# Performance work log

Hardware: AMD Instinct MI355X
Metric: run time of the kernel (lower is better)

## Reference

```python
import jax, jax.numpy as jnp
import numpy as np

K_STE = 10.0
T_STE = 0.1
BN_EPS = 1e-5


def binary_quantize(x):
    # forward of IR-Net BinaryQuantize: sign (sign(0)=0, matching torch.sign)
    return jnp.sign(x)


def setup_inputs() -> dict:
    key = jax.random.key(0)
    k1, k2, k3, k4 = jax.random.split(key, 4)
    B, Cin, Cout, H, W = 32, 256, 256, 56, 56
    x = jax.random.normal(k1, (B, Cin, H, W), dtype=jnp.float32)
    weight = jax.random.normal(k2, (Cout, Cin, 3, 3), dtype=jnp.float32) * 0.05
    gamma = jnp.ones((Cout,), dtype=jnp.float32)
    beta = jnp.zeros((Cout,), dtype=jnp.float32)
    running_mean = jax.random.normal(k3, (Cout,), dtype=jnp.float32) * 0.1
    running_var = jax.random.uniform(k4, (Cout,), dtype=jnp.float32, minval=0.5, maxval=1.5)
    return {"x": x, "weight": weight, "gamma": gamma, "beta": beta,
            "running_mean": running_mean, "running_var": running_var}


def reference(x, weight, gamma, beta, running_mean, running_var):
    stride = 1
    cout = weight.shape[0]
    wf = weight.reshape(cout, -1)                      # [Cout, Cin*3*3]
    n = wf.shape[1]
    mean = jnp.mean(wf, axis=1, keepdims=True)
    # torch std: unbiased (ddof=1)
    std = jnp.sqrt(jnp.sum((wf - mean) ** 2, axis=1, keepdims=True) / (n - 1))
    bw = (wf - mean) / std                             # standardized weights
    # detached per-channel power-of-two scale
    sw = jnp.exp2(jnp.round(jnp.log2(jnp.mean(jnp.abs(bw), axis=1))))  # [Cout]
    sw = jax.lax.stop_gradient(sw)
    bw = binary_quantize(bw).reshape(weight.shape) * sw[:, None, None, None]
    ba = binary_quantize(x)
    y = jax.lax.conv_general_dilated(
        ba, bw, window_strides=(stride, stride), padding=((1, 1), (1, 1)),
        dimension_numbers=("NCHW", "OIHW", "NCHW"))
    # BatchNorm2d (inference) + Hardtanh
    inv = gamma / jnp.sqrt(running_var + BN_EPS)
    y = y * inv[None, :, None, None] + (beta - running_mean * inv)[None, :, None, None]
    return jnp.clip(y, -1.0, 1.0)
```

## Files before the change

### kernel.cpp

```cpp
#include <hip/hip_runtime.h>
#include <hip/hip_bf16.h>
#include <cstdint>
#include <cstddef>


typedef int int4v __attribute__((ext_vector_type(4)));

#define CIN   256
#define COUT  256
#define SPAT  3136
#define SPAD  3364
#define BATCH 32
#define XHALF 32768

__global__ __launch_bounds__(256) void prep_kernel(
    const float* __restrict__ x, int8_t* __restrict__ xp,
    const float* __restrict__ wgt, const float* __restrict__ gamma,
    const float* __restrict__ beta, const float* __restrict__ rmean,
    const float* __restrict__ rvar, int8_t* __restrict__ wfrag,
    float* __restrict__ Sc, float* __restrict__ Tc) {
  const int bx  = blockIdx.x;
  const int by  = blockIdx.y;
  const int tid = threadIdx.x;

  if (bx < 49) {
    const int s0 = bx * 64;
    __shared__ uint8_t xt[64][272];
    const int g  = tid >> 6;
    const int si = tid & 63;
#pragma unroll
    for (int k = 0; k < 4; ++k) {
      const int cin16 = (g * 4 + k) * 16;
      const float* src = x + ((size_t)by * CIN + cin16) * SPAT + s0 + si;
      uint32_t w[4] = {0u, 0u, 0u, 0u};
#pragma unroll
      for (int e = 0; e < 16; ++e) {
        float v = src[(size_t)e * SPAT];
        uint32_t sb = (v > 0.f) ? 1u : ((v < 0.f) ? 0xFFu : 0u);
        w[e >> 2] |= sb << ((e & 3) * 8);
      }
      *(int4v*)&xt[si][cin16] = (int4v){(int)w[0], (int)w[1], (int)w[2], (int)w[3]};
    }
    __syncthreads();
    const int row = tid >> 2;
    const int sub = tid & 3;
    const int s = s0 + row;
    const int h = s / 56;
    int8_t* dst = xp + ((size_t)by * SPAD + (size_t)(s + 2 * h + 59)) * CIN + sub * 64;
#pragma unroll
    for (int j = 0; j < 4; ++j)
      *(int4v*)(dst + j * 16) = *(const int4v*)&xt[row][sub * 64 + j * 16];
    return;
  }

  if (bx == 49) {
    int8_t* xpb = xp + (size_t)by * SPAD * CIN;
    const int4v zz = (int4v){0, 0, 0, 0};
    for (int q = tid; q < 228 * 16; q += 256) {
      int p = q >> 4, c = q & 15;
      int pp;
      if (p < 58)       pp = p;
      else if (p < 116) pp = 57 * 58 + (p - 58);
      else if (p < 172) pp = (p - 116 + 1) * 58;
      else              pp = (p - 172 + 1) * 58 + 57;
      *(int4v*)(xpb + (size_t)pp * CIN + c * 16) = zz;
    }
    return;
  }

  const int co = (bx - 50) * 32 + by;
  __shared__ float red[256];
  const float* wc = wgt + (size_t)co * 2304;
  float v[9];
#pragma unroll
  for (int j = 0; j < 9; ++j) v[j] = wc[tid + j * 256];
  float s = 0.f;
#pragma unroll
  for (int j = 0; j < 9; ++j) s += v[j];
  red[tid] = s; __syncthreads();
#pragma unroll
  for (int o = 128; o > 0; o >>= 1) { if (tid < o) red[tid] += red[tid + o]; __syncthreads(); }
  const float mean = red[0] * (1.0f / 2304.0f);
  __syncthreads();
  float ss = 0.f, sa = 0.f;
#pragma unroll
  for (int j = 0; j < 9; ++j) {
    float d = v[j] - mean;
    ss += d * d;
    sa += fabsf(d);
  }
  red[tid] = ss; __syncthreads();
#pragma unroll
  for (int o = 128; o > 0; o >>= 1) { if (tid < o) red[tid] += red[tid + o]; __syncthreads(); }
  const float var_sum = red[0];
  __syncthreads();
  red[tid] = sa; __syncthreads();
#pragma unroll
  for (int o = 128; o > 0; o >>= 1) { if (tid < o) red[tid] += red[tid + o]; __syncthreads(); }
  const float abs_sum = red[0];
  const float stdv = sqrtf(var_sum / 2303.0f);
  const float mean_abs = abs_sum / (2304.0f * stdv);
  const float sw = exp2f(rintf(log2f(mean_abs)));

  const int z = co >> 7, row = co & 127;
  const int wv = row >> 6, m = (row >> 4) & 3, l15w = row & 15;
#pragma unroll
  for (int j = 0; j < 9; ++j) {
    int i = tid + j * 256;
    int cin = i / 9;
    int tap = i - cin * 9;
    float d = v[j] - mean;
    int8_t bits = (d > 0.f) ? (int8_t)1 : ((d < 0.f) ? (int8_t)-1 : (int8_t)0);
    int c0i = cin >> 7, cl = cin & 127;
    int chunk = cl >> 4;
    int kb = chunk >> 2, chp = chunk & 3, e = cl & 15;
    int lane = chp * 16 + l15w;
    int g = z * 18 + c0i * 9 + tap;
    size_t flat = (size_t)(g * 2 + wv) * 8192
                + (m * 2 + kb) * 1024 + lane * 16 + e;
    wfrag[flat] = bits;
  }
  if (tid == 0) {
    float inv = gamma[co] / sqrtf(rvar[co] + 1e-5f);
    Sc[co] = sw * inv;
    Tc[co] = beta[co] - rmean[co] * inv;
  }
}

__device__ __forceinline__ void gload_lds16(const void* g, void* l) {
  __builtin_amdgcn_global_load_lds(
      (const __attribute__((address_space(1))) uint32_t*)g,
      (__attribute__((address_space(3))) uint32_t*)l, 16, 0, 0);
}

__global__ __launch_bounds__(256, 2) void conv_kernel(
    const int8_t* __restrict__ xp, const int8_t* __restrict__ wfrag,
    const float* __restrict__ Sc, const float* __restrict__ Tc,
    float* __restrict__ out) {
  const int tile = blockIdx.x;
  const int b    = blockIdx.y;
  const int s0   = tile * 128;

  const int tid  = threadIdx.x;
  const int lane = tid & 63;
  const int wave = tid >> 6;
  const int wv   = wave >> 1;
  const int wco  = wv * 64;
  const int wp   = (wave & 1) * 64;
  const int l15  = lane & 15;
  const int chp  = lane >> 4;

  __shared__ uint8_t XsF[2 * XHALF];

  const int h0   = s0 / 56;
  const int base = s0 + 2 * h0;

  int offn[4];
#pragma unroll
  for (int n = 0; n < 4; ++n) {
    int s = s0 + wp + n * 16 + l15;
    int sc = s < SPAT ? s : SPAT - 1;
    int h = sc / 56;
    offn[n] = sc + 2 * h + 59 - base;
  }

  const int8_t* xb  = xp + (size_t)b * SPAD * CIN;
  const int8_t* wba = wfrag + (size_t)wv * 8192 + (size_t)lane * 16;

  auto issueX = [&](int bufi, int c0e) {
#pragma unroll
    for (int j = 0; j < 8; ++j) {
      int q   = j * 256 + tid;
      int row = q >> 3, c = q & 7;
      int gr  = base + row;
      if (gr > SPAD - 1) gr = SPAD - 1;
      gload_lds16(xb + (size_t)gr * CIN + c0e + ((c ^ (row & 7)) << 4),
                  XsF + bufi * XHALF + (q << 4));
    }
  };

  int4v af[2][8];
  auto loadAf = [&](int g, int buf) {
#pragma unroll
    for (int q8 = 0; q8 < 8; ++q8)
      af[buf][q8] = *(const int4v*)(wba + (size_t)g * 16384 + q8 * 1024);
  };

  int4v acc[4][4];
#pragma unroll
  for (int m = 0; m < 4; ++m)
#pragma unroll
    for (int n = 0; n < 4; ++n) acc[m][n] = (int4v){0, 0, 0, 0};

  issueX(0, 0);
  issueX(1, 128);
  loadAf(0, 0);
  __syncthreads();

#pragma unroll 1
  for (int z = 0; z < 2; ++z) {
    if (z) loadAf(18, 0);

#pragma unroll
    for (int s = 0; s < 18; ++s) {
      const int cur = s & 1;
      const int tap = s < 9 ? s : s - 9;
      const int tapoff = (tap / 3) * 58 + (tap - (tap / 3) * 3) - 59;
      const int hof = (s >= 9) ? XHALF : 0;

      if (s < 17) loadAf(z * 18 + s + 1, cur ^ 1);

#pragma unroll
      for (int kb = 0; kb < 2; ++kb) {
        int4v bf[4];
#pragma unroll
        for (int n = 0; n < 4; ++n) {
          int r = offn[n] + tapoff;
          bf[n] = *(const int4v*)(XsF + hof + (r << 7)
                                  + (((kb * 4 + chp) ^ (r & 7)) << 4));
        }
        __builtin_amdgcn_s_setprio(1);
#pragma unroll
        for (int m = 0; m < 4; ++m)
#pragma unroll
          for (int n = 0; n < 4; ++n)
            acc[m][n] = __builtin_amdgcn_mfma_i32_16x16x64_i8(
                af[cur][m * 2 + kb], bf[n], acc[m][n], 0, 0, 0);
        __builtin_amdgcn_s_setprio(0);
      }
    }

#pragma unroll
    for (int m = 0; m < 4; ++m) {
      const int cor0 = z * 128 + wco + m * 16 + chp * 4;
      float Sv[4], Tv[4];
#pragma unroll
      for (int r = 0; r < 4; ++r) { Sv[r] = Sc[cor0 + r]; Tv[r] = Tc[cor0 + r]; }
#pragma unroll
      for (int n = 0; n < 4; ++n) {
        const int s = s0 + wp + n * 16 + l15;
        if (s < SPAT) {
          float* op = out + ((size_t)b * COUT + cor0) * SPAT + s;
#pragma unroll
          for (int r = 0; r < 4; ++r) {
            float v = (float)acc[m][n][r] * Sv[r] + Tv[r];
            v = fminf(1.0f, fmaxf(-1.0f, v));
            op[(size_t)r * SPAT] = v;
          }
        }
      }
    }
    if (z == 0) {
#pragma unroll
      for (int m = 0; m < 4; ++m)
#pragma unroll
        for (int n = 0; n < 4; ++n) acc[m][n] = (int4v){0, 0, 0, 0};
    }
  }
}

extern "C" void kernel_launch(void* const* d_in, const int* in_sizes, int n_in,
                              void* d_out, int out_size, void* d_ws, size_t ws_size,
                              hipStream_t stream) {
  const float* x     = (const float*)d_in[0];
  const float* wgt   = (const float*)d_in[1];
  const float* gamma = (const float*)d_in[2];
  const float* beta  = (const float*)d_in[3];
  const float* rmean = (const float*)d_in[4];
  const float* rvar  = (const float*)d_in[5];
  float* out = (float*)d_out;

  int8_t* xp = (int8_t*)d_ws;
  const size_t xp_bytes = (size_t)BATCH * SPAD * CIN;
  int8_t* wfrag = xp + xp_bytes;
  const size_t wfrag_bytes = (size_t)2 * 294912;
  float* Sc = (float*)(wfrag + wfrag_bytes);
  float* Tc = Sc + COUT;

  prep_kernel<<<dim3(58, BATCH), 256, 0, stream>>>(x, xp, wgt, gamma, beta,
                                                   rmean, rvar, wfrag, Sc, Tc);
  conv_kernel<<<dim3(25, BATCH), 256, 0, stream>>>(xp, wfrag, Sc, Tc, out);
}
```

Measured before the change: 92.69 us.

## Split output channels across 8 waves instead of looping two channel halves

The conv kernel now launches 512 threads per block, with the 8 waves covering all 256 output channels at once. Before, 4 waves looped twice over halves of 128 channels each. The weight-fragment layout in the prep kernel is reorganised to index 4 wave groups per tap slice, and the two-pass z loop plus its accumulator reset are removed. The activation tile is loaded into LDS once and shared by twice as many waves, which should improve reuse and latency hiding. In exchange the block needs more registers and LDS per CU, which may cut resident blocks.

```diff
diff --git a/kernel.cpp b/kernel.cpp
--- a/kernel.cpp
+++ b/kernel.cpp
@@ -102,8 +102,7 @@
   const float mean_abs = abs_sum / (2304.0f * stdv);
   const float sw = exp2f(rintf(log2f(mean_abs)));
 
-  const int z = co >> 7, row = co & 127;
-  const int wv = row >> 6, m = (row >> 4) & 3, l15w = row & 15;
+  const int wv = co >> 6, m = (co >> 4) & 3, l15w = co & 15;
 #pragma unroll
   for (int j = 0; j < 9; ++j) {
     int i = tid + j * 256;
@@ -115,9 +114,8 @@
     int chunk = cl >> 4;
     int kb = chunk >> 2, chp = chunk & 3, e = cl & 15;
     int lane = chp * 16 + l15w;
-    int g = z * 18 + c0i * 9 + tap;
-    size_t flat = (size_t)(g * 2 + wv) * 8192
-                + (m * 2 + kb) * 1024 + lane * 16 + e;
+    int g = c0i * 9 + tap;
+    size_t flat = ((size_t)(g * 4 + wv) * 8 + (m * 2 + kb)) * 1024 + lane * 16 + e;
     wfrag[flat] = bits;
   }
   if (tid == 0) {
@@ -133,7 +131,7 @@
       (__attribute__((address_space(3))) uint32_t*)l, 16, 0, 0);
 }
 
-__global__ __launch_bounds__(256, 2) void conv_kernel(
+__global__ __launch_bounds__(512, 2) void conv_kernel(
     const int8_t* __restrict__ xp, const int8_t* __restrict__ wfrag,
     const float* __restrict__ Sc, const float* __restrict__ Tc,
     float* __restrict__ out) {
@@ -145,7 +143,6 @@
   const int lane = tid & 63;
   const int wave = tid >> 6;
   const int wv   = wave >> 1;
-  const int wco  = wv * 64;
   const int wp   = (wave & 1) * 64;
   const int l15  = lane & 15;
   const int chp  = lane >> 4;
@@ -167,15 +164,17 @@
   const int8_t* xb  = xp + (size_t)b * SPAD * CIN;
   const int8_t* wba = wfrag + (size_t)wv * 8192 + (size_t)lane * 16;
 
-  auto issueX = [&](int bufi, int c0e) {
+  auto issueX = [&]() {
 #pragma unroll
     for (int j = 0; j < 8; ++j) {
-      int q   = j * 256 + tid;
-      int row = q >> 3, c = q & 7;
+      int q   = j * 512 + tid;
+      int hf  = q >> 11;
+      int qq  = q & 2047;
+      int row = qq >> 3, c = qq & 7;
       int gr  = base + row;
       if (gr > SPAD - 1) gr = SPAD - 1;
-      gload_lds16(xb + (size_t)gr * CIN + c0e + ((c ^ (row & 7)) << 4),
-                  XsF + bufi * XHALF + (q << 4));
+      gload_lds16(xb + (size_t)gr * CIN + hf * 128 + ((c ^ (row & 7)) << 4),
+                  XsF + ((size_t)q << 4));
     }
   };
 
@@ -183,7 +182,7 @@
   auto loadAf = [&](int g, int buf) {
 #pragma unroll
     for (int q8 = 0; q8 < 8; ++q8)
-      af[buf][q8] = *(const int4v*)(wba + (size_t)g * 16384 + q8 * 1024);
+      af[buf][q8] = *(const int4v*)(wba + (size_t)g * 32768 + q8 * 1024);
   };
 
   int4v acc[4][4];
@@ -192,69 +191,57 @@
 #pragma unroll
     for (int n = 0; n < 4; ++n) acc[m][n] = (int4v){0, 0, 0, 0};
 
-  issueX(0, 0);
-  issueX(1, 128);
+  issueX();
   loadAf(0, 0);
   __syncthreads();
 
-#pragma unroll 1
-  for (int z = 0; z < 2; ++z) {
-    if (z) loadAf(18, 0);
-
-#pragma unroll
-    for (int s = 0; s < 18; ++s) {
-      const int cur = s & 1;
-      const int tap = s < 9 ? s : s - 9;
-      const int tapoff = (tap / 3) * 58 + (tap - (tap / 3) * 3) - 59;
-      const int hof = (s >= 9) ? XHALF : 0;
-
-      if (s < 17) loadAf(z * 18 + s + 1, cur ^ 1);
-
-#pragma unroll
-      for (int kb = 0; kb < 2; ++kb) {
-        int4v bf[4];
-#pragma unroll
-        for (int n = 0; n < 4; ++n) {
-          int r = offn[n] + tapoff;
-          bf[n] = *(const int4v*)(XsF + hof + (r << 7)
-                                  + (((kb * 4 + chp) ^ (r & 7)) << 4));
-        }
-        __builtin_amdgcn_s_setprio(1);
-#pragma unroll
-        for (int m = 0; m < 4; ++m)
-#pragma unroll
-          for (int n = 0; n < 4; ++n)
-            acc[m][n] = __builtin_amdgcn_mfma_i32_16x16x64_i8(
-                af[cur][m * 2 + kb], bf[n], acc[m][n], 0, 0, 0);
-        __builtin_amdgcn_s_setprio(0);
+#pragma unroll
+  for (int s = 0; s < 18; ++s) {
+    const int cur = s & 1;
+    const int tap = s < 9 ? s : s - 9;
+    const int tapoff = (tap / 3) * 58 + (tap - (tap / 3) * 3) - 59;
+    const int hof = (s >= 9) ? XHALF : 0;
+
+    if (s < 17) loadAf(s + 1, cur ^ 1);
+
+#pragma unroll
+    for (int kb = 0; kb < 2; ++kb) {
+      int4v bf[4];
+#pragma unroll
+      for (int n = 0; n < 4; ++n) {
+        int r = offn[n] + tapoff;
+        bf[n] = *(const int4v*)(XsF + hof + (r << 7)
+                                + (((kb * 4 + chp) ^ (r & 7)) << 4));
       }
-    }
-
-#pragma unroll
-    for (int m = 0; m < 4; ++m) {
-      const int cor0 = z * 128 + wco + m * 16 + chp * 4;
-      float Sv[4], Tv[4];
-#pragma unroll
-      for (int r = 0; r < 4; ++r) { Sv[r] = Sc[cor0 + r]; Tv[r] = Tc[cor0 + r]; }
-#pragma unroll
-      for (int n = 0; n < 4; ++n) {
-        const int s = s0 + wp + n * 16 + l15;
-        if (s < SPAT) {
-          float* op = out + ((size_t)b * COUT + cor0) * SPAT + s;
-#pragma unroll
-          for (int r = 0; r < 4; ++r) {
-            float v = (float)acc[m][n][r] * Sv[r] + Tv[r];
-            v = fminf(1.0f, fmaxf(-1.0f, v));
-            op[(size_t)r * SPAT] = v;
-          }
+      __builtin_amdgcn_s_setprio(1);
+#pragma unroll
+      for (int m = 0; m < 4; ++m)
+#pragma unroll
+        for (int n = 0; n < 4; ++n)
+          acc[m][n] = __builtin_amdgcn_mfma_i32_16x16x64_i8(
+              af[cur][m * 2 + kb], bf[n], acc[m][n], 0, 0, 0);
+      __builtin_amdgcn_s_setprio(0);
+    }
+  }
+
+#pragma unroll
+  for (int m = 0; m < 4; ++m) {
+    const int cor0 = wv * 64 + m * 16 + chp * 4;
+    float Sv[4], Tv[4];
+#pragma unroll
+    for (int r = 0; r < 4; ++r) { Sv[r] = Sc[cor0 + r]; Tv[r] = Tc[cor0 + r]; }
+#pragma unroll
+    for (int n = 0; n < 4; ++n) {
+      const int s = s0 + wp + n * 16 + l15;
+      if (s < SPAT) {
+        float* op = out + ((size_t)b * COUT + cor0) * SPAT + s;
+#pragma unroll
+        for (int r = 0; r < 4; ++r) {
+          float v = (float)acc[m][n][r] * Sv[r] + Tv[r];
+          v = fminf(1.0f, fmaxf(-1.0f, v));
+          op[(size_t)r * SPAT] = v;
         }
       }
-    }
-    if (z == 0) {
-#pragma unroll
-      for (int m = 0; m < 4; ++m)
-#pragma unroll
-        for (int n = 0; n < 4; ++n) acc[m][n] = (int4v){0, 0, 0, 0};
     }
   }
 }
@@ -273,11 +260,11 @@
   int8_t* xp = (int8_t*)d_ws;
   const size_t xp_bytes = (size_t)BATCH * SPAD * CIN;
   int8_t* wfrag = xp + xp_bytes;
-  const size_t wfrag_bytes = (size_t)2 * 294912;
+  const size_t wfrag_bytes = (size_t)18 * 4 * 8192;
   float* Sc = (float*)(wfrag + wfrag_bytes);
   float* Tc = Sc + COUT;
 
   prep_kernel<<<dim3(58, BATCH), 256, 0, stream>>>(x, xp, wgt, gamma, beta,
                                                    rmean, rvar, wfrag, Sc, Tc);
-  conv_kernel<<<dim3(25, BATCH), 256, 0, stream>>>(xp, wfrag, Sc, Tc, out);
-}
+  conv_kernel<<<dim3(25, BATCH), 512, 0, stream>>>(xp, wfrag, Sc, Tc, out);
+}
```

Result: slower. 98.11 us (+5.9%).
